# Performance work log

Hardware: AMD Instinct MI355X
Metric: run time of the kernel (lower is better)

Reference implementation:

```python
import jax, jax.numpy as jnp
import numpy as np

N = 57254   # num nodes == embedding vocab (hardcoded in module)
E = 916064  # num edges = N * avg_degree(16)
D = 128     # node_input_dim == node_hidden_dim
H = 8       # num_heads
O = D // H  # out_feats per head = 16
B, T = 64, 512


def setup_inputs() -> dict:
    key = jax.random.key(0)
    ks = jax.random.split(key, 13)
    f = lambda k, s: jax.random.normal(k, s, jnp.float32) * 0.05
    return {
        "emb": f(ks[0], (N, D)),
        "W0": f(ks[1], (D, H * O)), "al0": f(ks[2], (H, O)), "ar0": f(ks[3], (H, O)), "b0": f(ks[4], (H * O,)),
        "W1": f(ks[5], (D, H * O)), "al1": f(ks[6], (H, O)), "ar1": f(ks[7], (H, O)), "b1": f(ks[8], (H * O,)),
        "n_feat": jax.random.randint(ks[9], (N,), 0, N),
        "src": jax.random.randint(ks[10], (E,), 0, N),
        "dst": jax.random.randint(ks[11], (E,), 0, N),
        "x": jax.random.randint(ks[12], (B, T), 0, N),
    }


def _gat_layer(h, W, al, ar, b, src, dst, activate):
    # h: (N, D) -> z: (N, H, O)
    z = (h @ W).reshape(N, H, O)
    el = jnp.sum(z * al, axis=-1)            # (N, H)
    er = jnp.sum(z * ar, axis=-1)            # (N, H)
    e = jax.nn.leaky_relu(el[src] + er[dst], 0.2)  # (E, H) edge scores
    # segment softmax over incoming edges per destination node
    m = jax.ops.segment_max(e, dst, num_segments=N)   # (N, H)
    a = jnp.exp(e - m[dst])
    s = jax.ops.segment_sum(a, dst, num_segments=N)   # (N, H)
    alpha = a / s[dst]                                # (E, H)
    rst = jax.ops.segment_sum(alpha[:, :, None] * z[src], dst, num_segments=N)  # (N, H, O)
    # residual (identity since in_feats == H*O) + bias
    rst = rst + h.reshape(N, H, O) + b.reshape(1, H, O)
    if activate:
        rst = jax.nn.leaky_relu(rst, 0.01)  # F.leaky_relu default slope
    return rst.reshape(N, H * O)


def reference(emb, W0, al0, ar0, b0, W1, al1, ar1, b1, n_feat, src, dst, x):
    h = emb[n_feat]                                        # (N, D) embedding lookup
    h = _gat_layer(h, W0, al0, ar0, b0, src, dst, True)    # layer 0 (activation)
    h = _gat_layer(h, W1, al1, ar1, b1, src, dst, False)   # layer 1 (no activation)
    # F.normalize(p=2, eps=1e-5)
    nrm = jnp.sqrt(jnp.sum(h * h, axis=-1, keepdims=True))
    v = h / jnp.maximum(nrm, 1e-5)
    # broadcast-expand + flat index == direct gather of node embeddings
    return v[x]                                            # (B, T, D)
```

## Files before the change

### kernel.cpp

```cpp
#include <hip/hip_runtime.h>

#define N_NODES 57254
#define N_EDGES 916064
#define DIM 128
#define NHEAD 8
#define BT (64*512)
#define NBKT 224
#define NCHUNK 256
#define CHUNK 3579
#define LOG2E 1.4426950408889634f

typedef __attribute__((ext_vector_type(8))) short short8v;
typedef __attribute__((ext_vector_type(4))) float f32x4;
typedef __attribute__((ext_vector_type(2))) float f32x2;

#if defined(__has_builtin)
#  if __has_builtin(__builtin_amdgcn_cvt_pk_f32_fp8) && __has_builtin(__builtin_amdgcn_cvt_pk_fp8_f32)
#    define USE_FP8 1
#  endif
#endif
#ifndef USE_FP8
#  define USE_FP8 0
#endif

#define ZSCALE 16.0f
#define ZSCALE_INV (1.0f/16.0f)

static __device__ __forceinline__ unsigned short f2bf(float f){
  unsigned int b = __builtin_bit_cast(unsigned int, f);
  b += 0x7fffu + ((b >> 16) & 1u);
  return (unsigned short)(b >> 16);
}
static __device__ __forceinline__ float bf2f(unsigned short u){
  unsigned int b = ((unsigned int)u) << 16;
  return __builtin_bit_cast(float, b);
}
static __device__ __forceinline__ float lo16f(unsigned int zz){
  return __builtin_bit_cast(float, zz << 16);
}
static __device__ __forceinline__ float hi16f(unsigned int zz){
  return __builtin_bit_cast(float, zz & 0xffff0000u);
}

#if USE_FP8
#define ZB 1
static __device__ __forceinline__ void z_store(unsigned char* Zp, float v){
  unsigned u = (unsigned)__builtin_amdgcn_cvt_pk_fp8_f32(v*ZSCALE, v*ZSCALE, 0, false);
  *Zp = (unsigned char)(u & 0xffu);
}
static __device__ __forceinline__ f32x2 z_pair(unsigned short w){
  return __builtin_amdgcn_cvt_pk_f32_fp8((int)(unsigned)w, false);
}
#else
#define ZB 2
static __device__ __forceinline__ void z_store(unsigned char* Zp, float v){
  *(unsigned short*)Zp = f2bf(v);
}
static __device__ __forceinline__ f32x2 z_pair(unsigned zz){
  f32x2 r; r.x = lo16f(zz)*ZSCALE; r.y = hi16f(zz)*ZSCALE; return r;
}
#endif


__global__ __launch_bounds__(256) void p1hist(const int* __restrict__ dst,
                                              int* __restrict__ bh){
  __shared__ int h[NBKT];
  int t = threadIdx.x, c = blockIdx.x;
  if (t < NBKT) h[t] = 0;
  __syncthreads();
  int lo = c*CHUNK, hi = lo + CHUNK; if (hi > N_EDGES) hi = N_EDGES;
  for (int i = lo + t; i < hi; i += 256)
    atomicAdd(&h[((unsigned)dst[i]) >> 8], 1);
  __syncthreads();
  if (t < NBKT) bh[t*NCHUNK + c] = h[t];
}

__global__ void scan_partial(const int* __restrict__ in, int* __restrict__ out,
                             int* __restrict__ bsum, int n){
  __shared__ int sm[256];
  int tid = threadIdx.x;
  int i = blockIdx.x*256 + tid;
  int v = (i < n) ? in[i] : 0;
  sm[tid] = v;
  __syncthreads();
  #pragma unroll
  for (int d = 1; d < 256; d <<= 1){
    int add = (tid >= d) ? sm[tid - d] : 0;
    __syncthreads();
    sm[tid] += add;
    __syncthreads();
  }
  if (i < n) out[i] = sm[tid] - v;
  if (tid == 255) bsum[blockIdx.x] = sm[255];
}

__global__ void scan_add2(int* __restrict__ out, const int* __restrict__ bsum,
                          int nb, int n){
  __shared__ int sm[256];
  int t = threadIdx.x, b = blockIdx.x;
  sm[t] = (t < b && t < nb) ? bsum[t] : 0;
  __syncthreads();
  #pragma unroll
  for (int d = 128; d; d >>= 1){
    if (t < d) sm[t] += sm[t + d];
    __syncthreads();
  }
  int i = b*256 + t;
  if (i < n) out[i] += sm[0];
}

__global__ __launch_bounds__(256) void p1scat(const int* __restrict__ src,
                                              const int* __restrict__ dst,
                                              const int* __restrict__ bases,
                                              unsigned* __restrict__ ebuf){
  __shared__ unsigned stage[CHUNK];
  __shared__ short bkt_of[CHUNK];
  __shared__ int lh[256], smm[256], ls[NBKT+1], cur[NBKT], gb[NBKT];
  int t = threadIdx.x, c = blockIdx.x;
  lh[t] = 0;
  __syncthreads();
  int lo = c*CHUNK, hi = lo + CHUNK; if (hi > N_EDGES) hi = N_EDGES;
  int len = hi - lo;
  for (int i = lo + t; i < hi; i += 256)
    atomicAdd(&lh[((unsigned)dst[i]) >> 8], 1);
  __syncthreads();
  int v = lh[t];
  smm[t] = v;
  __syncthreads();
  #pragma unroll
  for (int d = 1; d < 256; d <<= 1){
    int add = (t >= d) ? smm[t - d] : 0;
    __syncthreads();
    smm[t] += add;
    __syncthreads();
  }
  if (t < NBKT){ ls[t] = smm[t] - v; cur[t] = smm[t] - v; gb[t] = bases[t*NCHUNK + c]; }
  if (t == 255) ls[NBKT] = smm[255];
  __syncthreads();
  if (t < NBKT){
    int e0 = ls[t], e1 = ls[t+1];
    for (int k = e0; k < e1; ++k) bkt_of[k] = (short)t;
  }
  __syncthreads();
  for (int i = lo + t; i < hi; i += 256){
    unsigned d = (unsigned)dst[i];
    int b = d >> 8;
    int pos = atomicAdd(&cur[b], 1);
    stage[pos] = (((unsigned)src[i]) << 16) | (d & 255u);
  }
  __syncthreads();
  for (int k = t; k < len; k += 256){
    int b = bkt_of[k];
    ebuf[gb[b] + (k - ls[b])] = stage[k];
  }
}

__global__ __launch_bounds__(256) void p2fine(const unsigned* __restrict__ ebuf,
                                              const int* __restrict__ bases,
                                              int* __restrict__ offs,
                                              int* __restrict__ pcnt,
                                              int* __restrict__ csr){
  __shared__ int cnt[256], sm[256], plo[256], cur[256];
  int t = threadIdx.x, b = blockIdx.x;
  int bstart = bases[b*NCHUNK];
  int bend   = (b < NBKT-1) ? bases[(b+1)*NCHUNK] : N_EDGES;
  int pbstart = bstart + b*1792;
  cnt[t] = 0;
  __syncthreads();
  for (int i = bstart + t; i < bend; i += 256)
    atomicAdd(&cnt[ebuf[i] & 255u], 1);
  __syncthreads();
  int v = cnt[t];
  int pv = (v + 7) & ~7;
  sm[t] = pv;
  __syncthreads();
  #pragma unroll
  for (int d = 1; d < 256; d <<= 1){
    int add = (t >= d) ? sm[t - d] : 0;
    __syncthreads();
    sm[t] += add;
    __syncthreads();
  }
  plo[t] = sm[t] - pv;
  cur[t] = pbstart + plo[t];
  int nlo = b*256;
  int nn  = N_NODES - nlo; if (nn > 256) nn = 256;
  if (t < nn){ offs[nlo + t] = pbstart + plo[t]; pcnt[nlo + t] = pv; }
  __syncthreads();
  for (int i = bstart + t; i < bend; i += 256){
    unsigned e = ebuf[i];
    int pos = atomicAdd(&cur[e & 255u], 1);
    csr[pos] = (int)(e >> 16);
  }
  __syncthreads();
  if (t < nn){
    int end = pbstart + plo[t] + pv;
    for (int k = cur[t]; k < end; ++k) csr[k] = N_NODES;
  }
}

__global__ void twt_kernel(const float* __restrict__ W0, const float* __restrict__ W1,
                           unsigned short* __restrict__ Wt0, unsigned short* __restrict__ Wt1){
  int t = blockIdx.x*256 + threadIdx.x;
  int which = t >> 14;
  int i = t & 16383;
  int c = i >> 7, k = i & 127;
  const float* W = which ? W1 : W0;
  unsigned short* Wt = which ? Wt1 : Wt0;
  Wt[i] = f2bf(W[k*128 + c]);
}

template<int MODE>
__global__ __launch_bounds__(256) void gemm_nt(
    const void* __restrict__ Av, const int* __restrict__ gidx,
    const unsigned short* __restrict__ Wt,
    unsigned char* __restrict__ Z,
    unsigned short* __restrict__ Hb)
{
  __shared__ unsigned short As[128*128];
  __shared__ unsigned short Bs[128*128];
  int t = threadIdx.x;
  int brow = blockIdx.x * 128;
  {
    int r = t >> 1, half = t & 1;
    int grow = brow + r;
    bool valid = grow < N_NODES;
    unsigned srcr = 0u;
    if (MODE == 0) srcr = valid ? (unsigned)gidx[grow] : 0u;
    #pragma unroll
    for (int j = 0; j < 8; ++j){
      int c = half*64 + j*8;
      short8v pk;
      if (MODE == 0){
        const float* arow = (const float*)Av + (size_t)srcr * DIM;
        float4 a0, a1;
        if (valid){ a0 = *(const float4*)(arow + c); a1 = *(const float4*)(arow + c + 4); }
        else { a0 = make_float4(0.f,0.f,0.f,0.f); a1 = a0; }
        pk[0]=(short)f2bf(a0.x); pk[1]=(short)f2bf(a0.y); pk[2]=(short)f2bf(a0.z); pk[3]=(short)f2bf(a0.w);
        pk[4]=(short)f2bf(a1.x); pk[5]=(short)f2bf(a1.y); pk[6]=(short)f2bf(a1.z); pk[7]=(short)f2bf(a1.w);
        if (valid) *(short8v*)(Hb + (unsigned)grow*128u + c) = pk;
      } else {
        const unsigned short* A = (const unsigned short*)Av;
        if (valid) pk = *(const short8v*)(A + (unsigned)grow*128u + c);
        else       pk = (short8v){0,0,0,0,0,0,0,0};
      }
      int byte = (r*256 + c*2) ^ ((r & 7) << 4);
      *(short8v*)((char*)As + byte) = pk;
    }
    int cc = t >> 1, khalf = t & 1;
    #pragma unroll
    for (int j = 0; j < 8; ++j){
      int k0 = khalf*64 + j*8;
      short8v w = *(const short8v*)(Wt + cc*128 + k0);
      int byte = (cc*256 + k0*2) ^ ((cc & 7) << 4);
      *(short8v*)((char*)Bs + byte) = w;
    }
  }
  __syncthreads();
  int w = t >> 6, lane = t & 63;
  f32x4 acc[2][8];
  #pragma unroll
  for (int m=0;m<2;m++)
    #pragma unroll
    for (int n=0;n<8;n++) acc[m][n] = (f32x4){0.f,0.f,0.f,0.f};
  #pragma unroll
  for (int kk = 0; kk < 4; ++kk){
    int ks = kk*32 + (lane>>4)*8;
    short8v a[2], b[8];
    #pragma unroll
    for (int m=0;m<2;m++){
      int row = w*32 + m*16 + (lane & 15);
      int byte = (row*256 + ks*2) ^ ((row & 7) << 4);
      a[m] = *(const short8v*)((const char*)As + byte);
    }
    #pragma unroll
    for (int n=0;n<8;n++){
      int col = n*16 + (lane & 15);
      int byte = (col*256 + ks*2) ^ ((col & 7) << 4);
      b[n] = *(const short8v*)((const char*)Bs + byte);
    }
    #pragma unroll
    for (int m=0;m<2;m++)
      #pragma unroll
      for (int n=0;n<8;n++)
        acc[m][n] = __builtin_amdgcn_mfma_f32_16x16x32_bf16(a[m], b[n], acc[m][n], 0, 0, 0);
  }
  #pragma unroll
  for (int m=0;m<2;m++){
    int row_base = brow + w*32 + m*16 + ((lane>>4)<<2);
    #pragma unroll
    for (int r=0;r<4;r++){
      int grow = row_base + r;
      if (grow < N_NODES){
        #pragma unroll
        for (int n=0;n<8;n++)
          z_store(Z + ((unsigned)grow*128u + n*16 + (lane&15))*ZB, acc[m][n][r]);
      }
    }
  }
}

__global__ void eler_kernel(const unsigned char* __restrict__ Z,
                            const float* __restrict__ al, const float* __restrict__ ar,
                            unsigned short* __restrict__ el, float* __restrict__ er)
{
  int t = blockIdx.x*256 + threadIdx.x;
  if (t >= N_NODES*NHEAD){
    if (t < (N_NODES+1)*NHEAD){ el[t] = 0xFF80u; er[t] = 0.f; }
    return;
  }
  int h = t & 7;
  const unsigned char* zp = Z + ((unsigned)(t>>3)*128u + h*16)*ZB;
  float zv[16];
#if USE_FP8
  uint4 zw = *(const uint4*)zp;
  f32x2 p;
  p = z_pair((unsigned short)(zw.x & 0xffffu));      zv[0]=p.x;  zv[1]=p.y;
  p = __builtin_amdgcn_cvt_pk_f32_fp8((int)zw.x, true);  zv[2]=p.x;  zv[3]=p.y;
  p = z_pair((unsigned short)(zw.y & 0xffffu));      zv[4]=p.x;  zv[5]=p.y;
  p = __builtin_amdgcn_cvt_pk_f32_fp8((int)zw.y, true);  zv[6]=p.x;  zv[7]=p.y;
  p = z_pair((unsigned short)(zw.z & 0xffffu));      zv[8]=p.x;  zv[9]=p.y;
  p = __builtin_amdgcn_cvt_pk_f32_fp8((int)zw.z, true);  zv[10]=p.x; zv[11]=p.y;
  p = z_pair((unsigned short)(zw.w & 0xffffu));      zv[12]=p.x; zv[13]=p.y;
  p = __builtin_amdgcn_cvt_pk_f32_fp8((int)zw.w, true);  zv[14]=p.x; zv[15]=p.y;
#else
  short8v z0 = *(const short8v*)(zp);
  short8v z1 = *(const short8v*)(zp + 16);
  #pragma unroll
  for (int o = 0; o < 8; ++o){ zv[o] = bf2f((unsigned short)z0[o])*ZSCALE; zv[8+o] = bf2f((unsigned short)z1[o])*ZSCALE; }
#endif
  float sl = 0.f, sr = 0.f;
  #pragma unroll
  for (int o = 0; o < 16; ++o){
    sl += zv[o] * al[h*16+o]; sr += zv[o] * ar[h*16+o];
  }
  el[t] = f2bf(sl*(ZSCALE_INV*LOG2E)); er[t] = sr*(ZSCALE_INV*LOG2E);
}

__global__ __launch_bounds__(256) void edge_agg(
    const unsigned char* __restrict__ Z, const unsigned short* __restrict__ el,
    const float* __restrict__ er, const int* __restrict__ offs,
    const int* __restrict__ pcnt, const int* __restrict__ csr,
    const unsigned short* __restrict__ Hin, const float* __restrict__ bias,
    unsigned short* __restrict__ Hout, int activate)
{
  int tid  = threadIdx.x;
  int lane = tid & 63;
  int n    = __builtin_amdgcn_readfirstlane((int)(blockIdx.x*4 + (tid >> 6)));
  if (n >= N_NODES) return;
  int head  = lane >> 3;
  int eslot = lane & 7;

  int lo = offs[n], pc = pcnt[n];
  float ern = er[(unsigned)n*8u + head];
  float acc0 = 0.f, acc1 = 0.f, sacc_p = 0.f;
  const unsigned lidx = (unsigned)(lane*2);

  for (int base = lo; base < lo + pc; base += 8){
    unsigned sv = (unsigned)csr[base + eslot];
    unsigned short zz[8];
    #pragma unroll
    for (int e = 0; e < 8; ++e){
      int se = csr[base + e];
      zz[e] = *(const unsigned short*)(Z + ((unsigned)se*128u + lidx)*ZB);
    }
    float x = bf2f(el[sv*8u + head]) + ern;
    x = fmaxf(x, 0.2f*x);
    float w = exp2f(x);
    sacc_p += w;
    int wi = __builtin_bit_cast(int, w);
#define SWZ_STEP(E) { \
      float we = __builtin_bit_cast(float, \
          __builtin_amdgcn_ds_swizzle(wi, 0x18 | ((E)<<5))); \
      f32x2 z = z_pair(zz[E]); \
      acc0 += we*z.x; \
      acc1 += we*z.y; }
    SWZ_STEP(0) SWZ_STEP(1) SWZ_STEP(2) SWZ_STEP(3)
    SWZ_STEP(4) SWZ_STEP(5) SWZ_STEP(6) SWZ_STEP(7)
#undef SWZ_STEP
  }
  float sacc = sacc_p;
  sacc += __shfl_xor(sacc, 1, 64);
  sacc += __shfl_xor(sacc, 2, 64);
  sacc += __shfl_xor(sacc, 4, 64);
  float inv = (pc > 0) ? (ZSCALE_INV / sacc) : 0.f;
  unsigned hv = *(const unsigned*)(Hin + (unsigned)n*128u + lidx);
  int d = lane*2;
  float r0 = acc0*inv + lo16f(hv) + bias[d];
  float r1 = acc1*inv + hi16f(hv) + bias[d+1];
  if (activate){
    r0 = (r0 > 0.f) ? r0 : 0.01f*r0;
    r1 = (r1 > 0.f) ? r1 : 0.01f*r1;
  }
  unsigned outv = ((unsigned)f2bf(r1) << 16) | (unsigned)f2bf(r0);
  *(unsigned*)(Hout + (unsigned)n*128u + lidx) = outv;
}

__global__ __launch_bounds__(256) void norm_gather(const unsigned short* __restrict__ H,
    const int* __restrict__ x, float* __restrict__ out)
{
  int row = blockIdx.x*4 + (threadIdx.x >> 6);
  if (row >= BT) return;
  int lane = threadIdx.x & 63;
  unsigned xi = (unsigned)x[row];
  unsigned hv = *(const unsigned*)(H + xi*128u + (unsigned)(lane*2));
  float v0 = lo16f(hv), v1 = hi16f(hv);
  float ss = v0*v0 + v1*v1;
  #pragma unroll
  for (int m = 32; m; m >>= 1) ss += __shfl_xor(ss, m, 64);
  float sc = 1.f / fmaxf(sqrtf(ss), 1e-5f);
  int d = lane*2;
  out[(size_t)row*128 + d]     = v0*sc;
  out[(size_t)row*128 + d + 1] = v1*sc;
}

extern "C" void kernel_launch(void* const* d_in, const int* in_sizes, int n_in,
                              void* d_out, int out_size, void* d_ws, size_t ws_size,
                              hipStream_t stream)
{
  const float* emb = (const float*)d_in[0];
  const float* W0  = (const float*)d_in[1];
  const float* al0 = (const float*)d_in[2];
  const float* ar0 = (const float*)d_in[3];
  const float* b0  = (const float*)d_in[4];
  const float* W1  = (const float*)d_in[5];
  const float* al1 = (const float*)d_in[6];
  const float* ar1 = (const float*)d_in[7];
  const float* b1  = (const float*)d_in[8];
  const int* n_feat = (const int*)d_in[9];
  const int* srcv = (const int*)d_in[10];
  const int* dstv = (const int*)d_in[11];
  const int* xv   = (const int*)d_in[12];
  float* out = (float*)d_out;

  const int CSR_PAD = N_EDGES + NBKT*1792;

  char* p = (char*)d_ws;
  auto alloc = [&](size_t b)->char*{ char* q = p; p += (b + 255) & ~(size_t)255; return q; };
  unsigned char*  Z   = (unsigned char*)alloc((size_t)(N_NODES+1)*128*ZB);
  unsigned short* H1b = (unsigned short*)alloc((size_t)N_NODES*128*2);
  unsigned short* Hb0 = (unsigned short*)alloc((size_t)N_NODES*128*2);
  int* offs  = (int*)alloc((size_t)N_NODES*4);
  int* pcnt  = (int*)alloc((size_t)N_NODES*4);
  int* csr   = (int*)alloc((size_t)CSR_PAD*4);
  unsigned* ebuf = (unsigned*)alloc((size_t)N_EDGES*4);
  int* bh    = (int*)alloc((size_t)NBKT*NCHUNK*4);
  int* bsum  = (int*)alloc(256*4);
  unsigned short* Wt0 = (unsigned short*)alloc(128*128*2);
  unsigned short* Wt1 = (unsigned short*)alloc(128*128*2);
  unsigned short* el = (unsigned short*)ebuf;
  float* er = (float*)(((char*)ebuf) + (((size_t)(N_NODES+1)*8*2 + 255) & ~(size_t)255));

  const int NSCAN = NBKT*NCHUNK;

  p1hist<<<NCHUNK, 256, 0, stream>>>(dstv, bh);
  scan_partial<<<NSCAN/256, 256, 0, stream>>>(bh, bh, bsum, NSCAN);
  scan_add2<<<NSCAN/256, 256, 0, stream>>>(bh, bsum, NSCAN/256, NSCAN);
  p1scat<<<NCHUNK, 256, 0, stream>>>(srcv, dstv, bh, ebuf);
  p2fine<<<NBKT, 256, 0, stream>>>(ebuf, bh, offs, pcnt, csr);

  twt_kernel<<<128, 256, 0, stream>>>(W0, W1, Wt0, Wt1);

  int gemm_grid = (N_NODES + 127)/128;
  int agg_grid  = (N_NODES + 3)/4;
  int eler_grid = ((N_NODES+1)*8 + 255)/256;

  gemm_nt<0><<<gemm_grid, 256, 0, stream>>>(emb, n_feat, Wt0, Z, Hb0);
  eler_kernel<<<eler_grid, 256, 0, stream>>>(Z, al0, ar0, el, er);
  edge_agg<<<agg_grid, 256, 0, stream>>>(Z, el, er, offs, pcnt, csr, Hb0, b0, H1b, 1);
  gemm_nt<1><<<gemm_grid, 256, 0, stream>>>(H1b, nullptr, Wt1, Z, nullptr);
  eler_kernel<<<eler_grid, 256, 0, stream>>>(Z, al1, ar1, el, er);
  edge_agg<<<agg_grid, 256, 0, stream>>>(Z, el, er, offs, pcnt, csr, H1b, b1, H1b, 0);
  norm_gather<<<(BT + 3)/4, 256, 0, stream>>>(H1b, xv, out);
}
```

Baseline: 160.3 us.

## Remap edge aggregation lanes to edge×head with vector row loads and transpose reduce

Edge aggregation now gives each lane one (edge, head) pair. The lane loads that head's 16 features with one 16-byte vector read, instead of eight lanes each gathering 2-byte pieces after a swizzle broadcast of the weights. Partial sums are combined with a butterfly transpose-reduce across the 8 edge slots, so each lane ends with two output features. The padding row of Z (index N_NODES, used by padded CSR slots) is now zeroed inside the weight-transpose kernel so that the new unconditional reads of padded sources are safe. The cost is 16 accumulator registers per lane and extra shuffles at the end.

```diff
diff --git a/kernel.cpp b/kernel.cpp
--- a/kernel.cpp
+++ b/kernel.cpp
@@ -200,14 +200,20 @@
 }
 
 __global__ void twt_kernel(const float* __restrict__ W0, const float* __restrict__ W1,
-                           unsigned short* __restrict__ Wt0, unsigned short* __restrict__ Wt1){
+                           unsigned short* __restrict__ Wt0, unsigned short* __restrict__ Wt1,
+                           unsigned char* __restrict__ Z){
   int t = blockIdx.x*256 + threadIdx.x;
-  int which = t >> 14;
-  int i = t & 16383;
-  int c = i >> 7, k = i & 127;
-  const float* W = which ? W1 : W0;
-  unsigned short* Wt = which ? Wt1 : Wt0;
-  Wt[i] = f2bf(W[k*128 + c]);
+  if (t < 32768){
+    int which = t >> 14;
+    int i = t & 16383;
+    int c = i >> 7, k = i & 127;
+    const float* W = which ? W1 : W0;
+    unsigned short* Wt = which ? Wt1 : Wt0;
+    Wt[i] = f2bf(W[k*128 + c]);
+  } else {
+    int i = t - 32768;
+    if (i < 128*ZB) Z[(size_t)N_NODES*128*ZB + i] = 0;
+  }
 }
 
 template<int MODE>
@@ -348,52 +354,92 @@
   int lane = tid & 63;
   int n    = __builtin_amdgcn_readfirstlane((int)(blockIdx.x*4 + (tid >> 6)));
   if (n >= N_NODES) return;
-  int head  = lane >> 3;
-  int eslot = lane & 7;
+  int h = lane >> 3;
+  int e = lane & 7;
 
   int lo = offs[n], pc = pcnt[n];
-  float ern = er[(unsigned)n*8u + head];
-  float acc0 = 0.f, acc1 = 0.f, sacc_p = 0.f;
-  const unsigned lidx = (unsigned)(lane*2);
+  float ern = er[(unsigned)n*8u + h];
+  float acc[16];
+  #pragma unroll
+  for (int j=0;j<16;++j) acc[j] = 0.f;
+  float sacc = 0.f;
 
   for (int base = lo; base < lo + pc; base += 8){
-    unsigned sv = (unsigned)csr[base + eslot];
-    unsigned short zz[8];
-    #pragma unroll
-    for (int e = 0; e < 8; ++e){
-      int se = csr[base + e];
-      zz[e] = *(const unsigned short*)(Z + ((unsigned)se*128u + lidx)*ZB);
-    }
-    float x = bf2f(el[sv*8u + head]) + ern;
+    unsigned s = (unsigned)csr[base + e];
+#if USE_FP8
+    uint4 zw = *(const uint4*)(Z + s*128u + (unsigned)(h*16));
+#else
+    const unsigned short* zr = (const unsigned short*)Z + s*128u + (unsigned)(h*16);
+    short8v zlo = *(const short8v*)zr;
+    short8v zhi = *(const short8v*)(zr + 8);
+#endif
+    float x = bf2f(el[s*8u + h]) + ern;
     x = fmaxf(x, 0.2f*x);
     float w = exp2f(x);
-    sacc_p += w;
-    int wi = __builtin_bit_cast(int, w);
-#define SWZ_STEP(E) { \
-      float we = __builtin_bit_cast(float, \
-          __builtin_amdgcn_ds_swizzle(wi, 0x18 | ((E)<<5))); \
-      f32x2 z = z_pair(zz[E]); \
-      acc0 += we*z.x; \
-      acc1 += we*z.y; }
-    SWZ_STEP(0) SWZ_STEP(1) SWZ_STEP(2) SWZ_STEP(3)
-    SWZ_STEP(4) SWZ_STEP(5) SWZ_STEP(6) SWZ_STEP(7)
-#undef SWZ_STEP
-  }
-  float sacc = sacc_p;
+    sacc += w;
+#if USE_FP8
+    f32x2 p;
+    p = __builtin_amdgcn_cvt_pk_f32_fp8((int)zw.x, false); acc[0] +=w*p.x; acc[1] +=w*p.y;
+    p = __builtin_amdgcn_cvt_pk_f32_fp8((int)zw.x, true ); acc[2] +=w*p.x; acc[3] +=w*p.y;
+    p = __builtin_amdgcn_cvt_pk_f32_fp8((int)zw.y, false); acc[4] +=w*p.x; acc[5] +=w*p.y;
+    p = __builtin_amdgcn_cvt_pk_f32_fp8((int)zw.y, true ); acc[6] +=w*p.x; acc[7] +=w*p.y;
+    p = __builtin_amdgcn_cvt_pk_f32_fp8((int)zw.z, false); acc[8] +=w*p.x; acc[9] +=w*p.y;
+    p = __builtin_amdgcn_cvt_pk_f32_fp8((int)zw.z, true ); acc[10]+=w*p.x; acc[11]+=w*p.y;
+    p = __builtin_amdgcn_cvt_pk_f32_fp8((int)zw.w, false); acc[12]+=w*p.x; acc[13]+=w*p.y;
+    p = __builtin_amdgcn_cvt_pk_f32_fp8((int)zw.w, true ); acc[14]+=w*p.x; acc[15]+=w*p.y;
+#else
+    #pragma unroll
+    for (int j=0;j<8;++j) acc[j]   += w * bf2f((unsigned short)zlo[j]) * ZSCALE;
+    #pragma unroll
+    for (int j=0;j<8;++j) acc[8+j] += w * bf2f((unsigned short)zhi[j]) * ZSCALE;
+#endif
+  }
+
+  float t8[8];
+  {
+    bool up = (e & 4) != 0;
+    #pragma unroll
+    for (int j=0;j<8;++j){
+      float keep = up ? acc[8+j] : acc[j];
+      float send = up ? acc[j]   : acc[8+j];
+      t8[j] = keep + __shfl_xor(send, 4, 64);
+    }
+  }
+  float u4[4];
+  {
+    bool up = (e & 2) != 0;
+    #pragma unroll
+    for (int j=0;j<4;++j){
+      float keep = up ? t8[4+j] : t8[j];
+      float send = up ? t8[j]   : t8[4+j];
+      u4[j] = keep + __shfl_xor(send, 2, 64);
+    }
+  }
+  float v0, v1;
+  {
+    bool up = (e & 1) != 0;
+    float k0 = up ? u4[2] : u4[0];
+    float s0 = up ? u4[0] : u4[2];
+    float k1 = up ? u4[3] : u4[1];
+    float s1 = up ? u4[1] : u4[3];
+    v0 = k0 + __shfl_xor(s0, 1, 64);
+    v1 = k1 + __shfl_xor(s1, 1, 64);
+  }
   sacc += __shfl_xor(sacc, 1, 64);
   sacc += __shfl_xor(sacc, 2, 64);
   sacc += __shfl_xor(sacc, 4, 64);
+
   float inv = (pc > 0) ? (ZSCALE_INV / sacc) : 0.f;
-  unsigned hv = *(const unsigned*)(Hin + (unsigned)n*128u + lidx);
+  unsigned hv = *(const unsigned*)(Hin + (unsigned)n*128u + (unsigned)(lane*2));
   int d = lane*2;
-  float r0 = acc0*inv + lo16f(hv) + bias[d];
-  float r1 = acc1*inv + hi16f(hv) + bias[d+1];
+  float r0 = v0*inv + lo16f(hv) + bias[d];
+  float r1 = v1*inv + hi16f(hv) + bias[d+1];
   if (activate){
     r0 = (r0 > 0.f) ? r0 : 0.01f*r0;
     r1 = (r1 > 0.f) ? r1 : 0.01f*r1;
   }
   unsigned outv = ((unsigned)f2bf(r1) << 16) | (unsigned)f2bf(r0);
-  *(unsigned*)(Hout + (unsigned)n*128u + lidx) = outv;
+  *(unsigned*)(Hout + (unsigned)n*128u + (unsigned)(lane*2)) = outv;
 }
 
 __global__ __launch_bounds__(256) void norm_gather(const unsigned short* __restrict__ H,
@@ -459,7 +505,7 @@
   p1scat<<<NCHUNK, 256, 0, stream>>>(srcv, dstv, bh, ebuf);
   p2fine<<<NBKT, 256, 0, stream>>>(ebuf, bh, offs, pcnt, csr);
 
-  twt_kernel<<<128, 256, 0, stream>>>(W0, W1, Wt0, Wt1);
+  twt_kernel<<<129, 256, 0, stream>>>(W0, W1, Wt0, Wt1, Z);
 
   int gemm_grid = (N_NODES + 127)/128;
   int agg_grid  = (N_NODES + 3)/4;
```

New measurement: 167.4 us. 4.4% more time.
